# Kernel tuning notes

Measured on AMD Instinct MI355X. Metric: run time of the kernel, lower is better.

## Reference

```python
import jax, jax.numpy as jnp
import numpy as np

DIM = 512
NUM_HEADS = 8
HEAD_DIM = DIM // NUM_HEADS
SCALE = HEAD_DIM ** -0.5


def setup_inputs() -> dict:
    key = jax.random.key(0)
    k1, k2, k3, k4 = jax.random.split(key, 4)
    B, C, N = 4, DIM, 2048
    x = jax.random.normal(k1, (B, C, N), dtype=jnp.float32)
    # Conv1d with kernel_size=1 == channel matmul; store weights as [out, in].
    w_qkv = jax.random.normal(k2, (3 * C, C), dtype=jnp.float32) * (C ** -0.5)
    w_proj = jax.random.normal(k3, (C, C), dtype=jnp.float32) * (C ** -0.5)
    b_proj = jax.random.normal(k4, (C,), dtype=jnp.float32) * 0.01
    return {"x": x, "w_qkv": w_qkv, "w_proj": w_proj, "b_proj": b_proj}


def reference(x, w_qkv, w_proj, b_proj):
    B, C, N = x.shape
    H, hd = NUM_HEADS, HEAD_DIM
    # qkv 1x1 conv: [B, 3C, N]
    qkv = jnp.einsum('oc,bcn->bon', w_qkv, x)
    # reshape to (B, H, 3*hd, N) then chunk along channel-within-head axis
    qkv = qkv.reshape(B, H, 3 * hd, N)
    q, k, v = jnp.split(qkv, 3, axis=2)  # each (B, H, hd, N)
    # attn = k^T @ q * scale  -> (B, H, N_k, N_q); softmax over LAST axis (queries),
    # faithfully matching the original module.
    attn = jnp.einsum('bhdi,bhdj->bhij', k, q) * SCALE
    attn = jax.nn.softmax(attn, axis=-1)
    # x = v @ attn -> (B, H, hd, N)
    out = jnp.einsum('bhdi,bhij->bhdj', v, attn)
    out = out.reshape(B, C, N)
    # proj 1x1 conv with bias
    out = jnp.einsum('oc,bcn->bon', w_proj, out) + b_proj[None, :, None]
    return out
```

## Files before the change

### kernel.cpp

```cpp
#include <hip/hip_runtime.h>
#include <hip/hip_bf16.h>
#include <math.h>

#define SEQ   2048
#define NB    4
#define CDIM  512
#define NHEAD 8
#define HD    64
#define SL    (0.125f * 1.4426950408889634f)

typedef __attribute__((ext_vector_type(8))) short short8;
typedef __attribute__((ext_vector_type(8))) _Float16 f16x8;
typedef __attribute__((ext_vector_type(4))) float f32x4;
typedef __attribute__((ext_vector_type(16))) float f32x16;

__device__ inline f32x16 mfma32(f16x8 a, f16x8 b, f32x16 c) {
    return __builtin_amdgcn_mfma_f32_32x32x16_f16(a, b, c, 0, 0, 0);
}
__device__ inline f32x4 mfmaB(short8 a, short8 b, f32x4 c) {
    return __builtin_amdgcn_mfma_f32_16x16x32_bf16(a, b, c, 0, 0, 0);
}

__device__ inline ushort bf16_rne(float f) {
    union { float f; unsigned u; } c; c.f = f;
    unsigned u = c.u + 0x7fffu + ((c.u >> 16) & 1u);
    return (ushort)(u >> 16);
}
__device__ inline float bf16_to_f(ushort h) {
    union { unsigned u; float f; } c; c.u = ((unsigned)h) << 16;
    return c.f;
}
__device__ inline unsigned pk2u(float a, float b) {
    auto p = __builtin_amdgcn_cvt_pkrtz(a, b);
    union { decltype(p) v; unsigned u; } c; c.v = p; return c.u;
}
__device__ inline float fexp2(float x) { return __builtin_amdgcn_exp2f(x); }

__device__ inline int swz_off(int row, int byte_in_row) {
    return row * 128 + (byte_in_row ^ ((((row & 7) ^ ((row >> 3) & 7))) << 4));
}
__device__ inline short8 fragB(const ushort* base, int row, int kbyte) {
    return *(const short8*)(base + (swz_off(row, kbyte) >> 1));
}
__device__ inline void stage128(ushort* dst, const ushort* src, int tid) {
    const int row = tid >> 1, half = tid & 1;
    const ushort* s = src + (size_t)row * 512 + half * 32;
    #pragma unroll
    for (int c = 0; c < 4; ++c) {
        short8 v = *(const short8*)(s + c * 8);
        *(short8*)(dst + (swz_off(row, half * 64 + c * 16) >> 1)) = v;
    }
}


__global__ __launch_bounds__(256)
void conv_w(const float* __restrict__ w1, const float* __restrict__ w2,
            ushort* __restrict__ w1h, ushort* __restrict__ w1l,
            ushort* __restrict__ w2h, ushort* __restrict__ w2l)
{
    const size_t NW1 = (size_t)3 * CDIM * CDIM;
    size_t i = ((size_t)blockIdx.x * 256 + threadIdx.x) * 8;
    const float* src; ushort *dh, *dl;
    if (i < NW1) { src = w1 + i; dh = w1h + i; dl = w1l + i; }
    else { size_t j = i - NW1; src = w2 + j; dh = w2h + j; dl = w2l + j; }
    float4 a = *(const float4*)src, b = *(const float4*)(src + 4);
    float f[8] = {a.x, a.y, a.z, a.w, b.x, b.y, b.z, b.w};
    short8 hv, lv;
    #pragma unroll
    for (int e = 0; e < 8; ++e) {
        ushort hi = bf16_rne(f[e]);
        hv[e] = (short)hi;
        lv[e] = (short)bf16_rne(f[e] - bf16_to_f(hi));
    }
    *(short8*)dh = hv; *(short8*)dl = lv;
}

__global__ __launch_bounds__(256)
void conv_x(const float* __restrict__ x, ushort* __restrict__ xh)
{
    __shared__ float T[64][65];
    const int n0 = blockIdx.x * 64, c0 = blockIdx.y * 64, b = blockIdx.z;
    const int t = threadIdx.x, r = t >> 2, q = t & 3;
    const float* src = x + ((size_t)b * CDIM + c0 + r) * SEQ + n0 + q * 16;
    #pragma unroll
    for (int c = 0; c < 4; ++c) {
        float4 v = *(const float4*)(src + c * 4);
        T[r][q * 16 + c * 4 + 0] = v.x; T[r][q * 16 + c * 4 + 1] = v.y;
        T[r][q * 16 + c * 4 + 2] = v.z; T[r][q * 16 + c * 4 + 3] = v.w;
    }
    __syncthreads();
    short8 hv[2];
    #pragma unroll
    for (int k = 0; k < 16; ++k)
        hv[k >> 3][k & 7] = (short)bf16_rne(T[q * 16 + k][r]);
    size_t o = ((size_t)b * SEQ + n0 + r) * CDIM + c0 + q * 16;
    *(short8*)(xh + o) = hv[0]; *(short8*)(xh + o + 8) = hv[1];
}

template<int MODE>
__global__ __launch_bounds__(256)
void gemm_sp(const ushort* __restrict__ A0, const ushort* __restrict__ A1, size_t sA,
             const ushort* __restrict__ B0, const ushort* __restrict__ B1, size_t sB,
             _Float16* __restrict__ qblk, _Float16* __restrict__ kblk,
             _Float16* __restrict__ vT,
             float* __restrict__ outp, const float* __restrict__ bias)
{
    const int bn = blockIdx.x * 128, bm = blockIdx.y * 128, bat = blockIdx.z;
    __shared__ __align__(16) ushort sA0[8192], sA1[8192], sB0[8192], sB1[8192];
    const int tid = threadIdx.x;
    const int w = tid >> 6, lane = tid & 63, l15 = lane & 15, g = lane >> 4;
    const int wm = w >> 1, wn = w & 1;
    const ushort* Ah = A0 + sA * bat + (size_t)bm * 512;
    const ushort* Al = (MODE == 1) ? A1 + sA * bat + (size_t)bm * 512 : nullptr;
    const ushort* Bh = B0 + sB * bat + (size_t)bn * 512;
    const ushort* Bl = B1 + sB * bat + (size_t)bn * 512;

    f32x4 acc[4][4] = {};

    for (int k0 = 0; k0 < 512; k0 += 64) {
        __syncthreads();
        stage128(sA0, Ah + k0, tid);
        if (MODE == 1) stage128(sA1, Al + k0, tid);
        stage128(sB0, Bh + k0, tid);
        stage128(sB1, Bl + k0, tid);
        __syncthreads();
        #pragma unroll
        for (int kh = 0; kh < 2; ++kh) {
            short8 bh[4], bl[4];
            #pragma unroll
            for (int nf = 0; nf < 4; ++nf) {
                bh[nf] = fragB(sB0, 64 * wn + 16 * nf + l15, kh * 64 + g * 16);
                bl[nf] = fragB(sB1, 64 * wn + 16 * nf + l15, kh * 64 + g * 16);
            }
            #pragma unroll
            for (int mf = 0; mf < 4; ++mf) {
                short8 ah = fragB(sA0, 64 * wm + 16 * mf + l15, kh * 64 + g * 16);
                #pragma unroll
                for (int nf = 0; nf < 4; ++nf) {
                    acc[mf][nf] = mfmaB(ah, bh[nf], acc[mf][nf]);
                    acc[mf][nf] = mfmaB(ah, bl[nf], acc[mf][nf]);
                }
                if (MODE == 1) {
                    short8 al = fragB(sA1, 64 * wm + 16 * mf + l15, kh * 64 + g * 16);
                    #pragma unroll
                    for (int nf = 0; nf < 4; ++nf)
                        acc[mf][nf] = mfmaB(al, bh[nf], acc[mf][nf]);
                }
            }
        }
    }

    if (MODE == 0) {
        #pragma unroll
        for (int nf = 0; nf < 4; ++nf) {
            const int c0 = bn + 64 * wn + 16 * nf;
            const int h = c0 / 192, rr = c0 % 192;
            if (rr < 128) {
                const float sc = (rr < 64) ? 1.0f : SL;
                const int dpr = (rr & 63) + l15;
                _Float16* blob = (rr < 64) ? qblk : kblk;
                _Float16* base = blob + (size_t)(bat * NHEAD + h) * (SEQ * 64)
                               + (dpr >> 4) * 512 + (((dpr >> 3) & 1) * 32) * 8
                               + (dpr & 7);
                #pragma unroll
                for (int mf = 0; mf < 4; ++mf)
                    #pragma unroll
                    for (int r = 0; r < 4; ++r) {
                        const int sj = bm + 64 * wm + 16 * mf + 4 * g + r;
                        base[(sj >> 5) * 2048 + (sj & 31) * 8] =
                            (_Float16)(acc[mf][nf][r] * sc);
                    }
            } else {
                _Float16* base = vT + ((size_t)(bat * NHEAD + h) * SEQ) * HD + (rr - 128) + l15;
                #pragma unroll
                for (int mf = 0; mf < 4; ++mf)
                    #pragma unroll
                    for (int r = 0; r < 4; ++r) {
                        const int sj = bm + 64 * wm + 16 * mf + 4 * g + r;
                        base[(size_t)sj * HD] = (_Float16)acc[mf][nf][r];
                    }
            }
        }
    } else {
        #pragma unroll
        for (int mf = 0; mf < 4; ++mf)
            #pragma unroll
            for (int r = 0; r < 4; ++r) {
                const int co = bm + 64 * wm + 16 * mf + 4 * g + r;
                const float bv = bias[co];
                float* base = outp + ((size_t)bat * CDIM + co) * SEQ + bn + 64 * wn + l15;
                #pragma unroll
                for (int nf = 0; nf < 4; ++nf)
                    base[16 * nf] = acc[mf][nf][r] + bv;
            }
    }
}

__global__ __launch_bounds__(256, 4)
void attn_pass1(const _Float16* __restrict__ qblk, const _Float16* __restrict__ kblk,
                float* __restrict__ cvals)
{
    const int ib = blockIdx.x, bh = blockIdx.y;
    const _Float16* qb = qblk + (size_t)bh * (SEQ * 64);
    const _Float16* kb = kblk + (size_t)bh * (SEQ * 64);
    const int tid = threadIdx.x, w = tid >> 6, lane = tid & 63;

    __shared__ float red[4][2][32];

    f16x8 kf[2][4];
    #pragma unroll
    for (int ch = 0; ch < 2; ++ch)
        #pragma unroll
        for (int ks = 0; ks < 4; ++ks)
            kf[ch][ks] = *(const f16x8*)(kb + (ib * 2 + ch) * 2048 + ks * 512 + lane * 8);

    float lsum[2] = {0.f, 0.f};

    for (int jc = w; jc < 64; jc += 4) {
        const _Float16* qc = qb + jc * 2048 + lane * 8;
        f16x8 q0 = *(const f16x8*)(qc);
        f16x8 q1 = *(const f16x8*)(qc + 512);
        f16x8 q2 = *(const f16x8*)(qc + 1024);
        f16x8 q3 = *(const f16x8*)(qc + 1536);
        #pragma unroll
        for (int ch = 0; ch < 2; ++ch) {
            f32x16 s = {};
            s = mfma32(q0, kf[ch][0], s);
            s = mfma32(q1, kf[ch][1], s);
            s = mfma32(q2, kf[ch][2], s);
            s = mfma32(q3, kf[ch][3], s);
            float t0 = 0.f;
            #pragma unroll
            for (int r = 0; r < 16; ++r) t0 += fexp2(s[r]);
            lsum[ch] += t0;
        }
    }

    lsum[0] += __shfl_xor(lsum[0], 32);
    lsum[1] += __shfl_xor(lsum[1], 32);
    if (lane < 32) { red[w][0][lane] = lsum[0]; red[w][1][lane] = lsum[1]; }
    __syncthreads();
    if (tid < 64) {
        const int ch = tid >> 5, l = tid & 31;
        float s = red[0][ch][l] + red[1][ch][l] + red[2][ch][l] + red[3][ch][l];
        cvals[(size_t)bh * SEQ + ib * 64 + tid] = -0.5f * log2f(s);
    }
}

__global__ __launch_bounds__(256)
void prescale_v(const _Float16* __restrict__ vT, const float* __restrict__ cvals,
                _Float16* __restrict__ vblk)
{
    __shared__ float T[64][65];
    const int i0 = blockIdx.x * 64, bh = blockIdx.y;
    const int t = threadIdx.x, r = t >> 2, q = t & 3;
    const float cf = exp2f(cvals[(size_t)bh * SEQ + i0 + r]);
    const _Float16* src = vT + ((size_t)bh * SEQ + i0 + r) * HD + q * 16;
    f16x8 a = *(const f16x8*)src, b = *(const f16x8*)(src + 8);
    #pragma unroll
    for (int k = 0; k < 8; ++k) {
        T[r][q * 16 + k]     = (float)a[k] * cf;
        T[r][q * 16 + 8 + k] = (float)b[k] * cf;
    }
    __syncthreads();
    f16x8 o0, o1;
    #pragma unroll
    for (int k = 0; k < 8; ++k) {
        o0[k] = (_Float16)T[q * 16 + k][r];
        o1[k] = (_Float16)T[q * 16 + 8 + k][r];
    }
    const int ic  = (i0 >> 5) + (q >> 1);
    const int ksp = q & 1;
    const int dh  = r >> 5;
    _Float16* dst = vblk + (size_t)bh * (SEQ * 64)
                  + ic * 2048 + ksp * 1024 + dh * 512 + (r & 31) * 8;
    *(f16x8*)(dst)       = o0;
    *(f16x8*)(dst + 256) = o1;
}

__global__ __launch_bounds__(256, 4)
void attn_pass2(const _Float16* __restrict__ qblk, const _Float16* __restrict__ kblk,
                const _Float16* __restrict__ vblk, const float* __restrict__ cvals,
                ushort* __restrict__ aoth, ushort* __restrict__ aotl)
{
    const int lb  = blockIdx.x;
    const int xcd = lb & 7;
    const int idx = lb >> 3;
    const int bh  = xcd * 4 + (idx & 3);
    const int jt  = idx >> 2;
    const int b = bh >> 3, h = bh & 7;
    const _Float16* qb = qblk + (size_t)bh * (SEQ * 64);
    const _Float16* kb = kblk + (size_t)bh * (SEQ * 64);
    const _Float16* vb = vblk + (size_t)bh * (SEQ * 64);
    const float* cp = cvals + (size_t)bh * SEQ;

    __shared__ float red[2][32][64];

    const int tid = threadIdx.x;
    const int w = tid >> 6, lane = tid & 63, l31 = lane & 31, hb = lane >> 5;
    const int j0w = jt * 32;

    const _Float16* qc = qb + jt * 2048 + lane * 8;
    f16x8 qf0 = *(const f16x8*)(qc);
    f16x8 qf1 = *(const f16x8*)(qc + 512);
    f16x8 qf2 = *(const f16x8*)(qc + 1024);
    f16x8 qf3 = *(const f16x8*)(qc + 1536);

    f32x16 oacc0 = {};
    f32x16 oacc1 = {};

    for (int ic = w * 16; ic < w * 16 + 16; ++ic) {
        const int i0 = ic * 32;
        const _Float16* kc = kb + ic * 2048 + lane * 8;
        f16x8 kf0 = *(const f16x8*)(kc);
        f16x8 kf1 = *(const f16x8*)(kc + 512);
        f16x8 kf2 = *(const f16x8*)(kc + 1024);
        f16x8 kf3 = *(const f16x8*)(kc + 1536);
        const _Float16* vc = vb + ic * 2048 + lane * 8;
        f16x8 v00 = *(const f16x8*)(vc);
        f16x8 v01 = *(const f16x8*)(vc + 512);
        f16x8 v10 = *(const f16x8*)(vc + 1024);
        f16x8 v11 = *(const f16x8*)(vc + 1536);
        const float* cq = cp + i0 + 4 * hb;
        float4 c0 = *(const float4*)(cq);
        float4 c1 = *(const float4*)(cq + 8);
        float4 c2 = *(const float4*)(cq + 16);
        float4 c3 = *(const float4*)(cq + 24);

        f32x16 s = {c0.x, c0.y, c0.z, c0.w, c1.x, c1.y, c1.z, c1.w,
                    c2.x, c2.y, c2.z, c2.w, c3.x, c3.y, c3.z, c3.w};
        s = mfma32(kf0, qf0, s);
        s = mfma32(kf1, qf1, s);
        s = mfma32(kf2, qf2, s);
        s = mfma32(kf3, qf3, s);

        unsigned pk0 = pk2u(fexp2(s[0]),  fexp2(s[1]));
        unsigned pk1 = pk2u(fexp2(s[2]),  fexp2(s[3]));
        unsigned pk2 = pk2u(fexp2(s[4]),  fexp2(s[5]));
        unsigned pk3 = pk2u(fexp2(s[6]),  fexp2(s[7]));
        unsigned pk4 = pk2u(fexp2(s[8]),  fexp2(s[9]));
        unsigned pk5 = pk2u(fexp2(s[10]), fexp2(s[11]));
        unsigned pk6 = pk2u(fexp2(s[12]), fexp2(s[13]));
        unsigned pk7 = pk2u(fexp2(s[14]), fexp2(s[15]));

        auto sA0 = __builtin_amdgcn_permlane32_swap(pk0, pk2, false, false);
        auto sB0 = __builtin_amdgcn_permlane32_swap(pk1, pk3, false, false);
        auto sA1 = __builtin_amdgcn_permlane32_swap(pk4, pk6, false, false);
        auto sB1 = __builtin_amdgcn_permlane32_swap(pk5, pk7, false, false);
        union PU { unsigned u[4]; f16x8 v; };
        PU pa0, pa1;
        pa0.u[0] = sA0[0]; pa0.u[1] = sB0[0]; pa0.u[2] = sA0[1]; pa0.u[3] = sB0[1];
        pa1.u[0] = sA1[0]; pa1.u[1] = sB1[0]; pa1.u[2] = sA1[1]; pa1.u[3] = sB1[1];

        oacc0 = mfma32(pa0.v, v00, oacc0);
        oacc0 = mfma32(pa1.v, v10, oacc0);
        oacc1 = mfma32(pa0.v, v01, oacc1);
        oacc1 = mfma32(pa1.v, v11, oacc1);
    }

    if (w & 1) {
        #pragma unroll
        for (int r = 0; r < 16; ++r) {
            red[w >> 1][r][lane]      = oacc0[r];
            red[w >> 1][r + 16][lane] = oacc1[r];
        }
    }
    __syncthreads();
    if (!(w & 1)) {
        #pragma unroll
        for (int r = 0; r < 16; ++r) {
            oacc0[r] += red[w >> 1][r][lane];
            oacc1[r] += red[w >> 1][r + 16][lane];
        }
    }
    __syncthreads();
    if (w == 2) {
        #pragma unroll
        for (int r = 0; r < 16; ++r) {
            red[0][r][lane]      = oacc0[r];
            red[0][r + 16][lane] = oacc1[r];
        }
    }
    __syncthreads();
    if (w == 0) {
        #pragma unroll
        for (int r = 0; r < 16; ++r) {
            oacc0[r] += red[0][r][lane];
            oacc1[r] += red[0][r + 16][lane];
        }
        #pragma unroll
        for (int r = 0; r < 16; ++r) {
            const int j = j0w + (r & 3) + 8 * (r >> 2) + 4 * hb;
            const size_t row = ((size_t)b * SEQ + j) * CDIM + h * HD + l31;
            float v0 = oacc0[r], v1 = oacc1[r];
            ushort h0 = bf16_rne(v0), h1 = bf16_rne(v1);
            aoth[row]      = h0;
            aoth[row + 32] = h1;
            aotl[row]      = bf16_rne(v0 - bf16_to_f(h0));
            aotl[row + 32] = bf16_rne(v1 - bf16_to_f(h1));
        }
    }
}

extern "C" void kernel_launch(void* const* d_in, const int* in_sizes, int n_in,
                              void* d_out, int out_size, void* d_ws, size_t ws_size,
                              hipStream_t stream)
{
    const float* x      = (const float*)d_in[0];
    const float* w_qkv  = (const float*)d_in[1];
    const float* w_proj = (const float*)d_in[2];
    const float* b_proj = (const float*)d_in[3];
    float* out = (float*)d_out;

    char* p = (char*)d_ws;
    auto alloc = [&](size_t bytes) { char* q = p; p += (bytes + 255) & ~(size_t)255; return q; };
    _Float16* qblk = (_Float16*)alloc((size_t)NB * NHEAD * SEQ * 64 * 2);
    _Float16* kblk = (_Float16*)alloc((size_t)NB * NHEAD * SEQ * 64 * 2);
    _Float16* vT   = (_Float16*)alloc((size_t)NB * NHEAD * SEQ * HD * 2);
    _Float16* vblk = (_Float16*)alloc((size_t)NB * NHEAD * SEQ * 64 * 2);
    float*    cvals = (float*)alloc((size_t)NB * NHEAD * SEQ * 4);
    ushort*   xTh  = (ushort*)alloc((size_t)NB * SEQ * CDIM * 2);
    ushort*   wqh  = (ushort*)alloc((size_t)3 * CDIM * CDIM * 2);
    ushort*   wql  = (ushort*)alloc((size_t)3 * CDIM * CDIM * 2);
    ushort*   wph  = (ushort*)alloc((size_t)CDIM * CDIM * 2);
    ushort*   wpl  = (ushort*)alloc((size_t)CDIM * CDIM * 2);
    ushort*   aoth = (ushort*)alloc((size_t)NB * SEQ * CDIM * 2);
    ushort*   aotl = (ushort*)alloc((size_t)NB * SEQ * CDIM * 2);

    dim3 blk(256);
    conv_w<<<dim3(512), blk, 0, stream>>>(w_qkv, w_proj, wqh, wql, wph, wpl);
    conv_x<<<dim3(SEQ / 64, CDIM / 64, NB), blk, 0, stream>>>(x, xTh);
    gemm_sp<0><<<dim3(12, 16, NB), blk, 0, stream>>>(
        xTh, nullptr, (size_t)SEQ * CDIM, wqh, wql, 0,
        qblk, kblk, vT, nullptr, nullptr);
    attn_pass1<<<dim3(SEQ / 64, NB * NHEAD), blk, 0, stream>>>(qblk, kblk, cvals);
    prescale_v<<<dim3(SEQ / 64, NB * NHEAD), blk, 0, stream>>>(vT, cvals, vblk);
    attn_pass2<<<dim3(2048), blk, 0, stream>>>(
        qblk, kblk, vblk, cvals, aoth, aotl);
    gemm_sp<1><<<dim3(16, 4, NB), blk, 0, stream>>>(
        wph, wpl, 0, aoth, aotl, (size_t)SEQ * CDIM,
        nullptr, nullptr, nullptr, out, b_proj);
}
```

Measured before the change: 160.3 us.

## Share K/V tiles across waves via double-buffered LDS in attention pass 2

attn_pass2 now gives each of the four waves its own 32-query tile, so a block covers 128 queries, and every wave sweeps all keys. Previously the four waves split the key range for a single 32-query tile and combined results through LDS. Each K/V chunk is loaded from global memory once per block into a double-buffered LDS tile that all waves reuse, with a barrier per iteration. This removes the cross-wave reduction and cuts global K/V traffic by four. In exchange the grid shrinks from 2048 to 512 blocks, occupancy drops, and each global load is stored to LDS right after issue, so its latency is not well hidden.

```diff
diff --git a/kernel.cpp b/kernel.cpp
--- a/kernel.cpp
+++ b/kernel.cpp
@@ -278,7 +278,7 @@
     *(f16x8*)(dst + 256) = o1;
 }
 
-__global__ __launch_bounds__(256, 4)
+__global__ __launch_bounds__(256, 2)
 void attn_pass2(const _Float16* __restrict__ qblk, const _Float16* __restrict__ kblk,
                 const _Float16* __restrict__ vblk, const float* __restrict__ cvals,
                 ushort* __restrict__ aoth, ushort* __restrict__ aotl)
@@ -294,34 +294,47 @@
     const _Float16* vb = vblk + (size_t)bh * (SEQ * 64);
     const float* cp = cvals + (size_t)bh * SEQ;
 
-    __shared__ float red[2][32][64];
+    __shared__ __align__(16) _Float16 KV[2][4096];
 
     const int tid = threadIdx.x;
     const int w = tid >> 6, lane = tid & 63, l31 = lane & 31, hb = lane >> 5;
-    const int j0w = jt * 32;
-
-    const _Float16* qc = qb + jt * 2048 + lane * 8;
+    const int j0w = jt * 128 + w * 32;
+
+    const _Float16* qc = qb + (size_t)(j0w >> 5) * 2048 + lane * 8;
     f16x8 qf0 = *(const f16x8*)(qc);
     f16x8 qf1 = *(const f16x8*)(qc + 512);
     f16x8 qf2 = *(const f16x8*)(qc + 1024);
     f16x8 qf3 = *(const f16x8*)(qc + 1536);
 
+    *(f16x8*)(&KV[0][tid * 8])        = *(const f16x8*)(kb + tid * 8);
+    *(f16x8*)(&KV[0][2048 + tid * 8]) = *(const f16x8*)(vb + tid * 8);
+    __syncthreads();
+
     f32x16 oacc0 = {};
     f32x16 oacc1 = {};
 
-    for (int ic = w * 16; ic < w * 16 + 16; ++ic) {
-        const int i0 = ic * 32;
-        const _Float16* kc = kb + ic * 2048 + lane * 8;
+    for (int ic = 0; ic < 64; ++ic) {
+        const _Float16* cur = &KV[ic & 1][0];
+        if (ic + 1 < 64) {
+            f16x8 kv = *(const f16x8*)(kb + (size_t)(ic + 1) * 2048 + tid * 8);
+            f16x8 vv = *(const f16x8*)(vb + (size_t)(ic + 1) * 2048 + tid * 8);
+            _Float16* nb = &KV[(ic + 1) & 1][0];
+            *(f16x8*)(nb + tid * 8)        = kv;
+            *(f16x8*)(nb + 2048 + tid * 8) = vv;
+        }
+
+        const _Float16* kc = cur + lane * 8;
         f16x8 kf0 = *(const f16x8*)(kc);
         f16x8 kf1 = *(const f16x8*)(kc + 512);
         f16x8 kf2 = *(const f16x8*)(kc + 1024);
         f16x8 kf3 = *(const f16x8*)(kc + 1536);
-        const _Float16* vc = vb + ic * 2048 + lane * 8;
+        const _Float16* vc = cur + 2048 + lane * 8;
         f16x8 v00 = *(const f16x8*)(vc);
         f16x8 v01 = *(const f16x8*)(vc + 512);
         f16x8 v10 = *(const f16x8*)(vc + 1024);
         f16x8 v11 = *(const f16x8*)(vc + 1536);
-        const float* cq = cp + i0 + 4 * hb;
+
+        const float* cq = cp + ic * 32 + 4 * hb;
         float4 c0 = *(const float4*)(cq);
         float4 c1 = *(const float4*)(cq + 8);
         float4 c2 = *(const float4*)(cq + 16);
@@ -356,49 +369,20 @@
         oacc0 = mfma32(pa1.v, v10, oacc0);
         oacc1 = mfma32(pa0.v, v01, oacc1);
         oacc1 = mfma32(pa1.v, v11, oacc1);
-    }
-
-    if (w & 1) {
-        #pragma unroll
-        for (int r = 0; r < 16; ++r) {
-            red[w >> 1][r][lane]      = oacc0[r];
-            red[w >> 1][r + 16][lane] = oacc1[r];
-        }
-    }
-    __syncthreads();
-    if (!(w & 1)) {
-        #pragma unroll
-        for (int r = 0; r < 16; ++r) {
-            oacc0[r] += red[w >> 1][r][lane];
-            oacc1[r] += red[w >> 1][r + 16][lane];
-        }
-    }
-    __syncthreads();
-    if (w == 2) {
-        #pragma unroll
-        for (int r = 0; r < 16; ++r) {
-            red[0][r][lane]      = oacc0[r];
-            red[0][r + 16][lane] = oacc1[r];
-        }
-    }
-    __syncthreads();
-    if (w == 0) {
-        #pragma unroll
-        for (int r = 0; r < 16; ++r) {
-            oacc0[r] += red[0][r][lane];
-            oacc1[r] += red[0][r + 16][lane];
-        }
-        #pragma unroll
-        for (int r = 0; r < 16; ++r) {
-            const int j = j0w + (r & 3) + 8 * (r >> 2) + 4 * hb;
-            const size_t row = ((size_t)b * SEQ + j) * CDIM + h * HD + l31;
-            float v0 = oacc0[r], v1 = oacc1[r];
-            ushort h0 = bf16_rne(v0), h1 = bf16_rne(v1);
-            aoth[row]      = h0;
-            aoth[row + 32] = h1;
-            aotl[row]      = bf16_rne(v0 - bf16_to_f(h0));
-            aotl[row + 32] = bf16_rne(v1 - bf16_to_f(h1));
-        }
+
+        __syncthreads();
+    }
+
+    #pragma unroll
+    for (int r = 0; r < 16; ++r) {
+        const int j = j0w + (r & 3) + 8 * (r >> 2) + 4 * hb;
+        const size_t row = ((size_t)b * SEQ + j) * CDIM + h * HD + l31;
+        float v0 = oacc0[r], v1 = oacc1[r];
+        ushort h0 = bf16_rne(v0), h1 = bf16_rne(v1);
+        aoth[row]      = h0;
+        aoth[row + 32] = h1;
+        aotl[row]      = bf16_rne(v0 - bf16_to_f(h0));
+        aotl[row + 32] = bf16_rne(v1 - bf16_to_f(h1));
     }
 }
 
@@ -435,7 +419,7 @@
         qblk, kblk, vT, nullptr, nullptr);
     attn_pass1<<<dim3(SEQ / 64, NB * NHEAD), blk, 0, stream>>>(qblk, kblk, cvals);
     prescale_v<<<dim3(SEQ / 64, NB * NHEAD), blk, 0, stream>>>(vT, cvals, vblk);
-    attn_pass2<<<dim3(2048), blk, 0, stream>>>(
+    attn_pass2<<<dim3(512), blk, 0, stream>>>(
         qblk, kblk, vblk, cvals, aoth, aotl);
     gemm_sp<1><<<dim3(16, 4, NB), blk, 0, stream>>>(
         wph, wpl, 0, aoth, aotl, (size_t)SEQ * CDIM,
```

After: 166.8 us. 1.04x slower.

## Process two query tiles per attn_pass2 block and XCD-swizzle attn_pass1 grid

Applied to the files above, without the earlier changes.

attn_pass2 now handles 64 query columns per block (two 32-wide tiles), so each K/V/c fragment loaded from memory is reused for two score/PV MFMA chains, and the grid is halved to 1024 blocks. This lowers K/V global traffic per unit of work but raises register pressure, so launch bounds drop to 3 blocks per SIMD. attn_pass1 switches to a 1D grid with an XCD-aware mapping so that blocks for the same batch-head land on the same XCD, which should improve L2 locality.

```diff
diff --git a/kernel.cpp b/kernel.cpp
--- a/kernel.cpp
+++ b/kernel.cpp
@@ -200,7 +200,10 @@
 void attn_pass1(const _Float16* __restrict__ qblk, const _Float16* __restrict__ kblk,
                 float* __restrict__ cvals)
 {
-    const int ib = blockIdx.x, bh = blockIdx.y;
+    const int lb = blockIdx.x;
+    const int xcd = lb & 7, idx = lb >> 3;
+    const int bh = xcd * 4 + (idx & 3);
+    const int ib = idx >> 2;
     const _Float16* qb = qblk + (size_t)bh * (SEQ * 64);
     const _Float16* kb = kblk + (size_t)bh * (SEQ * 64);
     const int tid = threadIdx.x, w = tid >> 6, lane = tid & 63;
@@ -278,7 +281,7 @@
     *(f16x8*)(dst + 256) = o1;
 }
 
-__global__ __launch_bounds__(256, 4)
+__global__ __launch_bounds__(256, 3)
 void attn_pass2(const _Float16* __restrict__ qblk, const _Float16* __restrict__ kblk,
                 const _Float16* __restrict__ vblk, const float* __restrict__ cvals,
                 ushort* __restrict__ aoth, ushort* __restrict__ aotl)
@@ -298,16 +301,21 @@
 
     const int tid = threadIdx.x;
     const int w = tid >> 6, lane = tid & 63, l31 = lane & 31, hb = lane >> 5;
-    const int j0w = jt * 32;
-
-    const _Float16* qc = qb + jt * 2048 + lane * 8;
-    f16x8 qf0 = *(const f16x8*)(qc);
-    f16x8 qf1 = *(const f16x8*)(qc + 512);
-    f16x8 qf2 = *(const f16x8*)(qc + 1024);
-    f16x8 qf3 = *(const f16x8*)(qc + 1536);
-
-    f32x16 oacc0 = {};
-    f32x16 oacc1 = {};
+    const int j0 = jt * 64;
+
+    const _Float16* qcA = qb + (size_t)(jt * 2) * 2048 + lane * 8;
+    f16x8 qf0 = *(const f16x8*)(qcA);
+    f16x8 qf1 = *(const f16x8*)(qcA + 512);
+    f16x8 qf2 = *(const f16x8*)(qcA + 1024);
+    f16x8 qf3 = *(const f16x8*)(qcA + 1536);
+    const _Float16* qcB = qcA + 2048;
+    f16x8 qg0 = *(const f16x8*)(qcB);
+    f16x8 qg1 = *(const f16x8*)(qcB + 512);
+    f16x8 qg2 = *(const f16x8*)(qcB + 1024);
+    f16x8 qg3 = *(const f16x8*)(qcB + 1536);
+
+    f32x16 oA0 = {}, oA1 = {};
+    f32x16 oB0 = {}, oB1 = {};
 
     for (int ic = w * 16; ic < w * 16 + 16; ++ic) {
         const int i0 = ic * 32;
@@ -326,73 +334,138 @@
         float4 c1 = *(const float4*)(cq + 8);
         float4 c2 = *(const float4*)(cq + 16);
         float4 c3 = *(const float4*)(cq + 24);
-
-        f32x16 s = {c0.x, c0.y, c0.z, c0.w, c1.x, c1.y, c1.z, c1.w,
-                    c2.x, c2.y, c2.z, c2.w, c3.x, c3.y, c3.z, c3.w};
-        s = mfma32(kf0, qf0, s);
-        s = mfma32(kf1, qf1, s);
-        s = mfma32(kf2, qf2, s);
-        s = mfma32(kf3, qf3, s);
-
-        unsigned pk0 = pk2u(fexp2(s[0]),  fexp2(s[1]));
-        unsigned pk1 = pk2u(fexp2(s[2]),  fexp2(s[3]));
-        unsigned pk2 = pk2u(fexp2(s[4]),  fexp2(s[5]));
-        unsigned pk3 = pk2u(fexp2(s[6]),  fexp2(s[7]));
-        unsigned pk4 = pk2u(fexp2(s[8]),  fexp2(s[9]));
-        unsigned pk5 = pk2u(fexp2(s[10]), fexp2(s[11]));
-        unsigned pk6 = pk2u(fexp2(s[12]), fexp2(s[13]));
-        unsigned pk7 = pk2u(fexp2(s[14]), fexp2(s[15]));
-
-        auto sA0 = __builtin_amdgcn_permlane32_swap(pk0, pk2, false, false);
-        auto sB0 = __builtin_amdgcn_permlane32_swap(pk1, pk3, false, false);
-        auto sA1 = __builtin_amdgcn_permlane32_swap(pk4, pk6, false, false);
-        auto sB1 = __builtin_amdgcn_permlane32_swap(pk5, pk7, false, false);
+        const f32x16 cinit = {c0.x, c0.y, c0.z, c0.w, c1.x, c1.y, c1.z, c1.w,
+                              c2.x, c2.y, c2.z, c2.w, c3.x, c3.y, c3.z, c3.w};
+
         union PU { unsigned u[4]; f16x8 v; };
-        PU pa0, pa1;
-        pa0.u[0] = sA0[0]; pa0.u[1] = sB0[0]; pa0.u[2] = sA0[1]; pa0.u[3] = sB0[1];
-        pa1.u[0] = sA1[0]; pa1.u[1] = sB1[0]; pa1.u[2] = sA1[1]; pa1.u[3] = sB1[1];
-
-        oacc0 = mfma32(pa0.v, v00, oacc0);
-        oacc0 = mfma32(pa1.v, v10, oacc0);
-        oacc1 = mfma32(pa0.v, v01, oacc1);
-        oacc1 = mfma32(pa1.v, v11, oacc1);
+
+        {
+            f32x16 s = cinit;
+            s = mfma32(kf0, qf0, s);
+            s = mfma32(kf1, qf1, s);
+            s = mfma32(kf2, qf2, s);
+            s = mfma32(kf3, qf3, s);
+            unsigned pk0 = pk2u(fexp2(s[0]),  fexp2(s[1]));
+            unsigned pk1 = pk2u(fexp2(s[2]),  fexp2(s[3]));
+            unsigned pk2 = pk2u(fexp2(s[4]),  fexp2(s[5]));
+            unsigned pk3 = pk2u(fexp2(s[6]),  fexp2(s[7]));
+            unsigned pk4 = pk2u(fexp2(s[8]),  fexp2(s[9]));
+            unsigned pk5 = pk2u(fexp2(s[10]), fexp2(s[11]));
+            unsigned pk6 = pk2u(fexp2(s[12]), fexp2(s[13]));
+            unsigned pk7 = pk2u(fexp2(s[14]), fexp2(s[15]));
+            auto sA0 = __builtin_amdgcn_permlane32_swap(pk0, pk2, false, false);
+            auto sB0 = __builtin_amdgcn_permlane32_swap(pk1, pk3, false, false);
+            auto sA1 = __builtin_amdgcn_permlane32_swap(pk4, pk6, false, false);
+            auto sB1 = __builtin_amdgcn_permlane32_swap(pk5, pk7, false, false);
+            PU pa0, pa1;
+            pa0.u[0] = sA0[0]; pa0.u[1] = sB0[0]; pa0.u[2] = sA0[1]; pa0.u[3] = sB0[1];
+            pa1.u[0] = sA1[0]; pa1.u[1] = sB1[0]; pa1.u[2] = sA1[1]; pa1.u[3] = sB1[1];
+            oA0 = mfma32(pa0.v, v00, oA0);
+            oA0 = mfma32(pa1.v, v10, oA0);
+            oA1 = mfma32(pa0.v, v01, oA1);
+            oA1 = mfma32(pa1.v, v11, oA1);
+        }
+        {
+            f32x16 s = cinit;
+            s = mfma32(kf0, qg0, s);
+            s = mfma32(kf1, qg1, s);
+            s = mfma32(kf2, qg2, s);
+            s = mfma32(kf3, qg3, s);
+            unsigned pk0 = pk2u(fexp2(s[0]),  fexp2(s[1]));
+            unsigned pk1 = pk2u(fexp2(s[2]),  fexp2(s[3]));
+            unsigned pk2 = pk2u(fexp2(s[4]),  fexp2(s[5]));
+            unsigned pk3 = pk2u(fexp2(s[6]),  fexp2(s[7]));
+            unsigned pk4 = pk2u(fexp2(s[8]),  fexp2(s[9]));
+            unsigned pk5 = pk2u(fexp2(s[10]), fexp2(s[11]));
+            unsigned pk6 = pk2u(fexp2(s[12]), fexp2(s[13]));
+            unsigned pk7 = pk2u(fexp2(s[14]), fexp2(s[15]));
+            auto sA0 = __builtin_amdgcn_permlane32_swap(pk0, pk2, false, false);
+            auto sB0 = __builtin_amdgcn_permlane32_swap(pk1, pk3, false, false);
+            auto sA1 = __builtin_amdgcn_permlane32_swap(pk4, pk6, false, false);
+            auto sB1 = __builtin_amdgcn_permlane32_swap(pk5, pk7, false, false);
+            PU pa0, pa1;
+            pa0.u[0] = sA0[0]; pa0.u[1] = sB0[0]; pa0.u[2] = sA0[1]; pa0.u[3] = sB0[1];
+            pa1.u[0] = sA1[0]; pa1.u[1] = sB1[0]; pa1.u[2] = sA1[1]; pa1.u[3] = sB1[1];
+            oB0 = mfma32(pa0.v, v00, oB0);
+            oB0 = mfma32(pa1.v, v10, oB0);
+            oB1 = mfma32(pa0.v, v01, oB1);
+            oB1 = mfma32(pa1.v, v11, oB1);
+        }
     }
 
     if (w & 1) {
         #pragma unroll
         for (int r = 0; r < 16; ++r) {
-            red[w >> 1][r][lane]      = oacc0[r];
-            red[w >> 1][r + 16][lane] = oacc1[r];
+            red[w >> 1][r][lane]      = oA0[r];
+            red[w >> 1][r + 16][lane] = oA1[r];
         }
     }
     __syncthreads();
     if (!(w & 1)) {
         #pragma unroll
         for (int r = 0; r < 16; ++r) {
-            oacc0[r] += red[w >> 1][r][lane];
-            oacc1[r] += red[w >> 1][r + 16][lane];
+            oA0[r] += red[w >> 1][r][lane];
+            oA1[r] += red[w >> 1][r + 16][lane];
         }
     }
     __syncthreads();
     if (w == 2) {
         #pragma unroll
         for (int r = 0; r < 16; ++r) {
-            red[0][r][lane]      = oacc0[r];
-            red[0][r + 16][lane] = oacc1[r];
+            red[0][r][lane]      = oA0[r];
+            red[0][r + 16][lane] = oA1[r];
         }
     }
     __syncthreads();
     if (w == 0) {
         #pragma unroll
         for (int r = 0; r < 16; ++r) {
-            oacc0[r] += red[0][r][lane];
-            oacc1[r] += red[0][r + 16][lane];
-        }
-        #pragma unroll
-        for (int r = 0; r < 16; ++r) {
-            const int j = j0w + (r & 3) + 8 * (r >> 2) + 4 * hb;
+            oA0[r] += red[0][r][lane];
+            oA1[r] += red[0][r + 16][lane];
+            const int j = j0 + (r & 3) + 8 * (r >> 2) + 4 * hb;
             const size_t row = ((size_t)b * SEQ + j) * CDIM + h * HD + l31;
-            float v0 = oacc0[r], v1 = oacc1[r];
+            float v0 = oA0[r], v1 = oA1[r];
+            ushort h0 = bf16_rne(v0), h1 = bf16_rne(v1);
+            aoth[row]      = h0;
+            aoth[row + 32] = h1;
+            aotl[row]      = bf16_rne(v0 - bf16_to_f(h0));
+            aotl[row + 32] = bf16_rne(v1 - bf16_to_f(h1));
+        }
+    }
+    __syncthreads();
+
+    if (w & 1) {
+        #pragma unroll
+        for (int r = 0; r < 16; ++r) {
+            red[w >> 1][r][lane]      = oB0[r];
+            red[w >> 1][r + 16][lane] = oB1[r];
+        }
+    }
+    __syncthreads();
+    if (!(w & 1)) {
+        #pragma unroll
+        for (int r = 0; r < 16; ++r) {
+            oB0[r] += red[w >> 1][r][lane];
+            oB1[r] += red[w >> 1][r + 16][lane];
+        }
+    }
+    __syncthreads();
+    if (w == 2) {
+        #pragma unroll
+        for (int r = 0; r < 16; ++r) {
+            red[0][r][lane]      = oB0[r];
+            red[0][r + 16][lane] = oB1[r];
+        }
+    }
+    __syncthreads();
+    if (w == 0) {
+        #pragma unroll
+        for (int r = 0; r < 16; ++r) {
+            oB0[r] += red[0][r][lane];
+            oB1[r] += red[0][r + 16][lane];
+            const int j = j0 + 32 + (r & 3) + 8 * (r >> 2) + 4 * hb;
+            const size_t row = ((size_t)b * SEQ + j) * CDIM + h * HD + l31;
+            float v0 = oB0[r], v1 = oB1[r];
             ushort h0 = bf16_rne(v0), h1 = bf16_rne(v1);
             aoth[row]      = h0;
             aoth[row + 32] = h1;
@@ -433,9 +506,9 @@
     gemm_sp<0><<<dim3(12, 16, NB), blk, 0, stream>>>(
         xTh, nullptr, (size_t)SEQ * CDIM, wqh, wql, 0,
         qblk, kblk, vT, nullptr, nullptr);
-    attn_pass1<<<dim3(SEQ / 64, NB * NHEAD), blk, 0, stream>>>(qblk, kblk, cvals);
+    attn_pass1<<<dim3(1024), blk, 0, stream>>>(qblk, kblk, cvals);
     prescale_v<<<dim3(SEQ / 64, NB * NHEAD), blk, 0, stream>>>(vT, cvals, vblk);
-    attn_pass2<<<dim3(2048), blk, 0, stream>>>(
+    attn_pass2<<<dim3(1024), blk, 0, stream>>>(
         qblk, kblk, vblk, cvals, aoth, aotl);
     gemm_sp<1><<<dim3(16, 4, NB), blk, 0, stream>>>(
         wph, wpl, 0, aoth, aotl, (size_t)SEQ * CDIM,
```

New measurement: 153.6 us. -4.2%, faster.
